# Kernel tuning notes

Measured on AMD Instinct MI355X. Metric: run time of the kernel, lower is better.

The kernel has to match this reference:

```python
import jax, jax.numpy as jnp
import numpy as np

TEMPERATURE = 0.07
BASE_TEMPERATURE = 0.07
EPS = 0.0001  # matches the +0.0001 in the torch code


def _l2norm(x):
    return x / jnp.clip(jnp.linalg.norm(x, axis=-1, keepdims=True), 1e-12, None)


def setup_inputs() -> dict:
    key = jax.random.key(0)
    k1, k2, k3 = jax.random.split(key, 3)
    # Sampled hard anchors: [total_classes=102, n_view=10, d=256], unit-norm
    # (original normalizes feats with F.normalize before _hard_anchor_sampling).
    X_anchor = _l2norm(jax.random.normal(k1, (102, 10, 256), dtype=jnp.float32))
    y_anchor = jax.random.randint(k2, (102,), 0, 19)
    # Memory queue of negatives: [class_num=19, cache_size=5000, d=256], unit-norm.
    queue = _l2norm(jax.random.normal(k3, (19, 5000, 256), dtype=jnp.float32))
    return {"X_anchor": X_anchor, "y_anchor": y_anchor, "queue": queue}


def reference(X_anchor, y_anchor, queue):
    anchor_num, n_view, d = X_anchor.shape
    class_num, cache_size, _ = queue.shape

    # anchor_feature = cat(unbind(X_anchor, dim=1), dim=0)  -> view-major order [n_view*anchor_num, d]
    anchor_feature = jnp.transpose(X_anchor, (1, 0, 2)).reshape(n_view * anchor_num, d)
    # _sample_negative flattens the queue class-major: [class_num*cache_size, d]
    contrast_feature = queue.reshape(class_num * cache_size, d)

    # mask = eq(y_anchor, y_contrast.T) then .repeat(anchor_count=n_view, contrast_count=1)
    y_a = jnp.tile(y_anchor, n_view)                                  # [N]
    y_c = jnp.repeat(jnp.arange(class_num, dtype=y_anchor.dtype), cache_size)  # [M]
    mask = (y_a[:, None] == y_c[None, :]).astype(X_anchor.dtype)      # [N, M]

    logits = jnp.matmul(anchor_feature, contrast_feature.T) / TEMPERATURE  # [N, M]
    logits_max = jax.lax.stop_gradient(jnp.max(logits, axis=1, keepdims=True))
    logits = logits - logits_max

    exp_logits = jnp.exp(logits)
    neg_sum = jnp.sum(exp_logits * (1.0 - mask), axis=1, keepdims=True)  # [N, 1]
    log_prob = logits - jnp.log(exp_logits + neg_sum)

    mean_log_prob_pos = jnp.sum(mask * log_prob, axis=1) / (jnp.sum(mask, axis=1) + EPS)
    loss = -(TEMPERATURE / BASE_TEMPERATURE) * mean_log_prob_pos
    return jnp.mean(loss)
```

## Files before the change

### kernel.cpp

```cpp
#include <hip/hip_runtime.h>
#include <hip/hip_bf16.h>
#include <stdint.h>

#define NCLS   19
#define CACHE  5000
#define NTILE  313
#define DDIM   256
#define NANCH  102
#define NVIEW  10
#define NROWS  1020
#define NSUB   13
#define NCHUNK (NCLS*NSUB)
#define NWG    (4*NCHUNK)
#define SCALE_A 20.6099319733f
#define LN2     0.69314718056f

using bf16x8 = __attribute__((ext_vector_type(8))) __bf16;
using f32x4  = __attribute__((ext_vector_type(4))) float;
using u16x8  = __attribute__((ext_vector_type(8))) unsigned short;

#if __has_builtin(__builtin_amdgcn_exp2f)
#define EXP2(x) __builtin_amdgcn_exp2f(x)
#else
#define EXP2(x) __expf((x) * LN2)
#endif

static __device__ __forceinline__ unsigned short f2bf(float x) {
    unsigned int u = __float_as_uint(x);
    unsigned int r = (u + 0x7FFFu + ((u >> 16) & 1u)) >> 16;
    return (unsigned short)r;
}

__global__ __launch_bounds__(256) void conv_queue2(const float* __restrict__ Qf,
                                                   unsigned short* __restrict__ Qbf) {
    int i = blockIdx.x * 256 + threadIdx.x;
    int lane = i & 63;
    int kk   = (i >> 6) & 7;
    int tile = i >> 9;
    int cls  = tile / NTILE;
    int t    = tile - cls * NTILE;
    int lm = lane & 15, lg = lane >> 4;
    int cic = t * 16 + lm;
    int k   = kk * 32 + lg * 8;
    u16x8 o;
    if (cic < CACHE) {
        const float* src = Qf + ((size_t)cls * CACHE + cic) * DDIM + k;
        float4 v0 = *reinterpret_cast<const float4*>(src);
        float4 v1 = *reinterpret_cast<const float4*>(src + 4);
        o[0]=f2bf(v0.x); o[1]=f2bf(v0.y); o[2]=f2bf(v0.z); o[3]=f2bf(v0.w);
        o[4]=f2bf(v1.x); o[5]=f2bf(v1.y); o[6]=f2bf(v1.z); o[7]=f2bf(v1.w);
    } else {
        for (int q = 0; q < 8; ++q) o[q] = 0;
    }
    *reinterpret_cast<u16x8*>(Qbf + (size_t)i * 8) = o;
}

__global__ __launch_bounds__(256) void conv_anchor2(const float* __restrict__ X,
                                                    unsigned short* __restrict__ Abf) {
    int n = blockIdx.x;
    int k = threadIdx.x;
    float v = 0.f;
    if (n < NROWS) {
        int vv = n / NANCH, a = n - vv * NANCH;
        v = X[((size_t)a * NVIEW + vv) * DDIM + k] * SCALE_A;
    }
    Abf[(size_t)n * DDIM + k] = f2bf(v);
}

__global__ __launch_bounds__(256, 2) void pass1_kernel(
    const unsigned short* __restrict__ Abf, const unsigned short* __restrict__ Qbf,
    const int* __restrict__ y,
    float* __restrict__ Pt, float* __restrict__ Pe, float* __restrict__ Ps)
{
    int orig = blockIdx.x;
    int xcd = orig & 7, slot = orig >> 3;
    int wid = (xcd < 4 ? xcd * 124 : 496 + (xcd - 4) * 123) + slot;
    int rt = wid & 3;
    int cs = wid >> 2;
    int cls = cs / NSUB;
    int sub = cs - cls * NSUB;
    int t0 = (NTILE * sub) / NSUB, t1 = (NTILE * (sub + 1)) / NSUB;

    int tid = threadIdx.x;
    int wave = tid >> 6, lane = tid & 63;
    int lg = lane >> 4, lm = lane & 15;
    int wrb = rt * 256 + wave * 64;

    bf16x8 afrag[4][8];
    #pragma unroll
    for (int f = 0; f < 4; ++f)
        #pragma unroll
        for (int kk = 0; kk < 8; ++kk)
            afrag[f][kk] = *reinterpret_cast<const bf16x8*>(
                Abf + (size_t)(wrb + f * 16 + lm) * DDIM + kk * 32 + lg * 8);

    float tacc[4][4] = {}, sacc[4][4] = {};

    const bf16x8* qchunk = reinterpret_cast<const bf16x8*>(Qbf) + (size_t)cls * NTILE * 512 + lane;

#define LOADB(dst, t) do {                                                    \
        const bf16x8* _p = qchunk + (size_t)(t) * 512;                        \
        _Pragma("unroll")                                                     \
        for (int kk = 0; kk < 8; ++kk) dst[kk] = _p[kk * 64];                 \
    } while (0)

#define COMPUTE(bf) do {                                                      \
        f32x4 acc[4];                                                         \
        _Pragma("unroll")                                                     \
        for (int f = 0; f < 4; ++f) acc[f] = (f32x4){0.f, 0.f, 0.f, 0.f};     \
        _Pragma("unroll")                                                     \
        for (int kk = 0; kk < 8; ++kk)                                        \
            _Pragma("unroll")                                                 \
            for (int f = 0; f < 4; ++f)                                       \
                acc[f] = __builtin_amdgcn_mfma_f32_16x16x32_bf16(             \
                    afrag[f][kk], bf[kk], acc[f], 0, 0, 0);                   \
        _Pragma("unroll")                                                     \
        for (int f = 0; f < 4; ++f)                                           \
            _Pragma("unroll")                                                 \
            for (int r = 0; r < 4; ++r) {                                     \
                float v = acc[f][r];                         \
                tacc[f][r] += EXP2(v);              \
                sacc[f][r] += v;                                              \
            }                                                                 \
    } while (0)

    bf16x8 bA[8], bB[8];
    int nt = t1 - t0;
    int it = 0;
    LOADB(bA, t0);
    for (;;) {
        if (it + 1 < nt) LOADB(bB, t0 + it + 1);
        COMPUTE(bA);
        ++it; if (it == nt) break;
        if (it + 1 < nt) LOADB(bA, t0 + it + 1);
        COMPUTE(bB);
        ++it; if (it == nt) break;
    }
#undef LOADB
#undef COMPUTE

    #pragma unroll
    for (int f = 0; f < 4; ++f)
        #pragma unroll
        for (int r = 0; r < 4; ++r) {
            float t = tacc[f][r], s = sacc[f][r];
            #pragma unroll
            for (int m = 1; m < 16; m <<= 1) {
                t += __shfl_xor(t, m);
                s += __shfl_xor(s, m);
            }
            if (lm == 0) {
                int row = wrb + f * 16 + lg * 4 + r;
                float mp = (row < NROWS && y[row % NANCH] == cls) ? 1.0f : 0.0f;
                size_t idx = (size_t)cs * 1024 + row;
                Pt[idx] = t; Pe[idx] = mp * t; Ps[idx] = mp * s;
            }
        }
}

__global__ __launch_bounds__(256) void reduce_rows(const float* __restrict__ Pt,
                                                   const float* __restrict__ Pe,
                                                   const float* __restrict__ Ps,
                                                   float* __restrict__ rowloss) {
    int tid = threadIdx.x;
    int row = blockIdx.x * 64 + (tid >> 2);
    int part = tid & 3;
    float tot = 0.f, pe = 0.f, ps = 0.f;
    for (int c = part; c < NCHUNK; c += 4) {
        size_t idx = (size_t)c * 1024 + row;
        tot += Pt[idx]; pe += Pe[idx]; ps += Ps[idx];
    }
    tot += __shfl_xor(tot, 1); pe += __shfl_xor(pe, 1); ps += __shfl_xor(ps, 1);
    tot += __shfl_xor(tot, 2); pe += __shfl_xor(pe, 2); ps += __shfl_xor(ps, 2);
    if (part == 0) {
        float r = 0.f;
        if (row < NROWS) {
            float ns    = tot - pe - 144.0f;
            float pos_e = pe - 8.0f;
            float pos_s = ps * LN2;
            float sum_logprob = pos_s - (5000.0f * logf(ns) + pos_e / ns);
            r = -sum_logprob / (5000.0f + 1e-4f);
        }
        rowloss[row] = r;
    }
}

__global__ __launch_bounds__(256) void pass3_kernel(const float* __restrict__ rowloss,
                                                    float* __restrict__ out) {
    float local = 0.f;
    for (int n = threadIdx.x; n < 1024; n += 256) local += rowloss[n];
    #pragma unroll
    for (int m = 1; m < 64; m <<= 1) local += __shfl_xor(local, m);
    __shared__ float sb[4];
    if ((threadIdx.x & 63) == 0) sb[threadIdx.x >> 6] = local;
    __syncthreads();
    if (threadIdx.x == 0)
        out[0] = (sb[0] + sb[1] + sb[2] + sb[3]) * (1.0f / (float)NROWS);
}

extern "C" void kernel_launch(void* const* d_in, const int* in_sizes, int n_in,
                              void* d_out, int out_size, void* d_ws, size_t ws_size,
                              hipStream_t stream) {
    const float* X  = (const float*)d_in[0];
    const int*   y  = (const int*)d_in[1];
    const float* Qf = (const float*)d_in[2];
    float* out = (float*)d_out;

    char* ws = (char*)d_ws;
    unsigned short* Qbf = (unsigned short*)(ws);
    unsigned short* Abf = (unsigned short*)(ws + 48717824);
    float* Pt      = (float*)(ws + 49242112);
    float* Pe      = (float*)(ws + 50253824);
    float* Ps      = (float*)(ws + 51265536);
    float* rowloss = (float*)(ws + 52277248);

    conv_queue2<<<11894, 256, 0, stream>>>(Qf, Qbf);
    conv_anchor2<<<1024, 256, 0, stream>>>(X, Abf);
    pass1_kernel<<<NWG, 256, 0, stream>>>(Abf, Qbf, y, Pt, Pe, Ps);
    reduce_rows<<<16, 256, 0, stream>>>(Pt, Pe, Ps, rowloss);
    pass3_kernel<<<1, 256, 0, stream>>>(rowloss, out);
}
```

Measured before the change: 112.9 us.

## Fuse queue bf16 conversion into the GEMM pass, reading fp32 directly

Removes the separate kernel that converted the whole fp32 queue to a bf16 tiled buffer. The main pass now loads fp32 queue rows directly, converts them to bf16 in registers, and zero-masks out-of-range columns. This avoids writing and re-reading an intermediate buffer, at the cost of more fp32 bytes per tile, less contiguous loads and extra conversion instructions in the hot loop.

```diff
diff --git a/kernel.cpp b/kernel.cpp
--- a/kernel.cpp
+++ b/kernel.cpp
@@ -17,7 +17,6 @@
 
 using bf16x8 = __attribute__((ext_vector_type(8))) __bf16;
 using f32x4  = __attribute__((ext_vector_type(4))) float;
-using u16x8  = __attribute__((ext_vector_type(8))) unsigned short;
 
 #if __has_builtin(__builtin_amdgcn_exp2f)
 #define EXP2(x) __builtin_amdgcn_exp2f(x)
@@ -29,30 +28,6 @@
     unsigned int u = __float_as_uint(x);
     unsigned int r = (u + 0x7FFFu + ((u >> 16) & 1u)) >> 16;
     return (unsigned short)r;
-}
-
-__global__ __launch_bounds__(256) void conv_queue2(const float* __restrict__ Qf,
-                                                   unsigned short* __restrict__ Qbf) {
-    int i = blockIdx.x * 256 + threadIdx.x;
-    int lane = i & 63;
-    int kk   = (i >> 6) & 7;
-    int tile = i >> 9;
-    int cls  = tile / NTILE;
-    int t    = tile - cls * NTILE;
-    int lm = lane & 15, lg = lane >> 4;
-    int cic = t * 16 + lm;
-    int k   = kk * 32 + lg * 8;
-    u16x8 o;
-    if (cic < CACHE) {
-        const float* src = Qf + ((size_t)cls * CACHE + cic) * DDIM + k;
-        float4 v0 = *reinterpret_cast<const float4*>(src);
-        float4 v1 = *reinterpret_cast<const float4*>(src + 4);
-        o[0]=f2bf(v0.x); o[1]=f2bf(v0.y); o[2]=f2bf(v0.z); o[3]=f2bf(v0.w);
-        o[4]=f2bf(v1.x); o[5]=f2bf(v1.y); o[6]=f2bf(v1.z); o[7]=f2bf(v1.w);
-    } else {
-        for (int q = 0; q < 8; ++q) o[q] = 0;
-    }
-    *reinterpret_cast<u16x8*>(Qbf + (size_t)i * 8) = o;
 }
 
 __global__ __launch_bounds__(256) void conv_anchor2(const float* __restrict__ X,
@@ -68,7 +43,7 @@
 }
 
 __global__ __launch_bounds__(256, 2) void pass1_kernel(
-    const unsigned short* __restrict__ Abf, const unsigned short* __restrict__ Qbf,
+    const unsigned short* __restrict__ Abf, const float* __restrict__ Qf,
     const int* __restrict__ y,
     float* __restrict__ Pt, float* __restrict__ Pe, float* __restrict__ Ps)
 {
@@ -96,12 +71,26 @@
 
     float tacc[4][4] = {}, sacc[4][4] = {};
 
-    const bf16x8* qchunk = reinterpret_cast<const bf16x8*>(Qbf) + (size_t)cls * NTILE * 512 + lane;
+    const float* qf = Qf + (size_t)cls * CACHE * DDIM + lg * 8;
 
 #define LOADB(dst, t) do {                                                    \
-        const bf16x8* _p = qchunk + (size_t)(t) * 512;                        \
-        _Pragma("unroll")                                                     \
-        for (int kk = 0; kk < 8; ++kk) dst[kk] = _p[kk * 64];                 \
+        int _colb = (t) * 16 + lm;                                            \
+        int _col  = _colb < CACHE ? _colb : CACHE - 1;                        \
+        bool _ok  = _colb < CACHE;                                            \
+        const float* _q = qf + (size_t)_col * DDIM;                           \
+        _Pragma("unroll")                                                     \
+        for (int kk = 0; kk < 8; ++kk) {                                      \
+            f32x4 _u0 = *reinterpret_cast<const f32x4*>(_q + kk * 32);        \
+            f32x4 _u1 = *reinterpret_cast<const f32x4*>(_q + kk * 32 + 4);    \
+            bf16x8 _b;                                                        \
+            _Pragma("unroll")                                                 \
+            for (int j = 0; j < 4; ++j) {                                     \
+                _b[j]     = (__bf16)_u0[j];                                   \
+                _b[j + 4] = (__bf16)_u1[j];                                   \
+            }                                                                 \
+            bf16x8 _z = {};                                                   \
+            dst[kk] = _ok ? _b : _z;                                          \
+        }                                                                     \
     } while (0)
 
 #define COMPUTE(bf) do {                                                      \
@@ -207,16 +196,14 @@
     float* out = (float*)d_out;
 
     char* ws = (char*)d_ws;
-    unsigned short* Qbf = (unsigned short*)(ws);
-    unsigned short* Abf = (unsigned short*)(ws + 48717824);
-    float* Pt      = (float*)(ws + 49242112);
-    float* Pe      = (float*)(ws + 50253824);
-    float* Ps      = (float*)(ws + 51265536);
-    float* rowloss = (float*)(ws + 52277248);
-
-    conv_queue2<<<11894, 256, 0, stream>>>(Qf, Qbf);
+    unsigned short* Abf = (unsigned short*)(ws);
+    float* Pt      = (float*)(ws + 524288);
+    float* Pe      = (float*)(ws + 1536000);
+    float* Ps      = (float*)(ws + 2547712);
+    float* rowloss = (float*)(ws + 3559424);
+
     conv_anchor2<<<1024, 256, 0, stream>>>(X, Abf);
-    pass1_kernel<<<NWG, 256, 0, stream>>>(Abf, Qbf, y, Pt, Pe, Ps);
+    pass1_kernel<<<NWG, 256, 0, stream>>>(Abf, Qf, y, Pt, Pe, Ps);
     reduce_rows<<<16, 256, 0, stream>>>(Pt, Pe, Ps, rowloss);
     pass3_kernel<<<1, 256, 0, stream>>>(rowloss, out);
 }
```

Result: slower. 230.1 us (+103.8%).
